# Performance work log

Hardware: AMD Instinct MI355X
Metric: run time of the kernel (lower is better)

The kernel has to match this reference:

```python
import jax, jax.numpy as jnp
import numpy as np

T, B, V, L = 512, 32, 512, 128
NEG = -1e9  # safe -inf surrogate (keeps logaddexp gradients finite)


def setup_inputs() -> dict:
    key = jax.random.key(0)
    k1, k2, k3 = jax.random.split(key, 3)
    log_probs = jax.nn.log_softmax(
        jax.random.normal(k1, (T, B, V), dtype=jnp.float32), axis=-1)
    # ASG transition parameter (init ones in the module; use small noise for a
    # non-degenerate reference). transition[i, j] = score of j -> i.
    transition = 0.1 * jax.random.normal(k2, (V, V), dtype=jnp.float32)
    targets = jax.random.randint(k3, (B, L), 0, V)
    input_lengths = jnp.full((B,), T, dtype=jnp.int32)
    target_lengths = jnp.full((B,), L, dtype=jnp.int32)
    return {"log_probs": log_probs, "transition": transition,
            "targets": targets, "input_lengths": input_lengths,
            "target_lengths": target_lengths}


def _fcc(log_probs, transition, input_lengths):
    """Fully-connected criterion: log-partition over all label paths. [B]"""
    def step(alpha, lp_t):  # alpha, lp_t: [B, V]
        # alpha'[b, i] = lp_t[b, i] + logsumexp_j(alpha[b, j] + trans[i, j])
        alpha = lp_t + jax.nn.logsumexp(
            alpha[:, None, :] + transition[None, :, :], axis=2)
        return alpha, jax.nn.logsumexp(alpha, axis=1)

    a0 = log_probs[0]
    _, tail = jax.lax.scan(step, a0, log_probs[1:])
    scores = jnp.concatenate(
        [jax.nn.logsumexp(a0, axis=1)[None], tail], axis=0)  # [T, B]
    return scores[input_lengths - 1, jnp.arange(scores.shape[1])]


def _fac(log_probs, transition, targets, input_lengths, target_lengths):
    """Forced-alignment criterion: DP constrained to the target label seq. [B]"""
    Tt, Bb, _ = log_probs.shape
    Ll = targets.shape[1]
    trans_self = transition[targets, targets]                    # [B, L] stay
    trans_prev = transition[targets[:, 1:], targets[:, :-1]]     # [B, L-1] advance
    # emit[t, b, s] = log_probs[t, b, targets[b, s]]
    emit = jnp.take_along_axis(
        log_probs, jnp.broadcast_to(targets[None], (Tt, Bb, Ll)), axis=2)

    sel = (target_lengths - 1)[:, None]  # [B, 1]

    def final_of(beta):
        return jnp.take_along_axis(beta, sel, axis=1)[:, 0]

    beta0 = jnp.where(jnp.arange(Ll)[None, :] == 0, emit[0], NEG)  # [B, L]

    def step(beta, em_t):
        stay = beta + trans_self
        move = jnp.concatenate(
            [jnp.full((Bb, 1), NEG, beta.dtype),
             beta[:, :-1] + trans_prev], axis=1)
        beta = em_t + jnp.logaddexp(stay, move)
        return beta, final_of(beta)

    _, tail = jax.lax.scan(step, beta0, emit[1:])
    fins = jnp.concatenate([final_of(beta0)[None], tail], axis=0)  # [T, B]
    return fins[input_lengths - 1, jnp.arange(Bb)]


def reference(log_probs, transition, targets, input_lengths, target_lengths):
    # ASG loss (reduction='none'): FCC - FAC, shape [B]
    fcc = _fcc(log_probs, transition, input_lengths)
    fac = _fac(log_probs, transition, targets, input_lengths, target_lengths)
    return fcc - fac
```

## Files before the change

kernel.cpp:

```cpp
#include <hip/hip_runtime.h>
#include <stdint.h>

#define T_ 512
#define B_ 32
#define V_ 512
#define L_ 128
#define NEGF (-1000000000.0f)

#define SE_Q 69.0f
#define SU_Q 127.0f
#define LOGC 9.078313f

template <int CTRL>
__device__ __forceinline__ int dppmov(int old_, int src) {
    return __builtin_amdgcn_update_dpp(old_, src, CTRL, 0xF, 0xF, false);
}
__device__ __forceinline__ float wave_max64(float x) {
    int xi = __float_as_int(x);
    x = fmaxf(x, __int_as_float(dppmov<0x111>(xi, xi))); xi = __float_as_int(x);
    x = fmaxf(x, __int_as_float(dppmov<0x112>(xi, xi))); xi = __float_as_int(x);
    x = fmaxf(x, __int_as_float(dppmov<0x114>(xi, xi))); xi = __float_as_int(x);
    x = fmaxf(x, __int_as_float(dppmov<0x118>(xi, xi))); xi = __float_as_int(x);
    x = fmaxf(x, __int_as_float(dppmov<0x142>(xi, xi))); xi = __float_as_int(x);
    x = fmaxf(x, __int_as_float(dppmov<0x143>(xi, xi)));
    return x;
}
__device__ __forceinline__ float wave_sum64(float x) {
    int xi = __float_as_int(x);
    x = x + __int_as_float(dppmov<0x111>(xi, xi)); xi = __float_as_int(x);
    x = x + __int_as_float(dppmov<0x112>(xi, xi)); xi = __float_as_int(x);
    x = x + __int_as_float(dppmov<0x114>(xi, xi)); xi = __float_as_int(x);
    x = x + __int_as_float(dppmov<0x118>(xi, xi)); xi = __float_as_int(x);
    x = x + __int_as_float(dppmov<0x142>(xi, xi)); xi = __float_as_int(x);
    x = x + __int_as_float(dppmov<0x143>(xi, xi));
    return x;
}
__device__ __forceinline__ unsigned fkey(float f) {
    unsigned u = __float_as_uint(f);
    return (u & 0x80000000u) ? ~u : (u | 0x80000000u);
}
__device__ __forceinline__ float funkey(unsigned k) {
    unsigned u = (k & 0x80000000u) ? (k ^ 0x80000000u) : ~k;
    return __uint_as_float(u);
}

__device__ __forceinline__ int gl_of(int lane) { return (lane & 3) | ((lane >> 1) & 4); }
__device__ __forceinline__ int g_of(int lane)  { return ((lane >> 2) & 1) | ((lane >> 3) & 6); }

__global__ void asg_prep(const float* __restrict__ trans, uint32_t* __restrict__ Et) {
    int o = blockIdx.x * blockDim.x + threadIdx.x;
    int d   = o & 3;
    int tid = (o >> 2) & 511;
    int q   = o >> 11;
    int w = tid >> 6, lane = tid & 63;
    int g = g_of(lane), gl = gl_of(lane);
    int c = q >> 2, kk = q & 3;
    int kp = (kk + (gl >> 1)) & 3;
    int m  = 4 * kp + d;
    int row = 64 * w + 8 * g + c;
    int j0  = 4 * (16 * gl + m);
    const float* tp = trans + (size_t)row * V_ + j0;
    uint32_t q0 = (uint32_t)fminf(127.0f, __expf(tp[0]) * SE_Q + 0.5f);
    uint32_t q1 = (uint32_t)fminf(127.0f, __expf(tp[1]) * SE_Q + 0.5f);
    uint32_t q2 = (uint32_t)fminf(127.0f, __expf(tp[2]) * SE_Q + 0.5f);
    uint32_t q3 = (uint32_t)fminf(127.0f, __expf(tp[3]) * SE_Q + 0.5f);
    Et[(size_t)o] = q0 | (q1 << 8) | (q2 << 16) | (q3 << 24);
}

__global__ __attribute__((amdgpu_flat_work_group_size(512, 512),
                          amdgpu_waves_per_eu(2, 2)))
void asg_main(
    const float* __restrict__ lp, const uint32_t* __restrict__ Et,
    const float* __restrict__ trans, const int* __restrict__ targets,
    const int* __restrict__ ilen, const int* __restrict__ tlen,
    float* __restrict__ fcc_ws, float* __restrict__ fac_ws)
{
    __shared__ float    facb[256];
    __shared__ __align__(16) uint32_t u_lds[128];
    __shared__ unsigned mslot[2];
    __shared__ float    sumf;

    const int bb  = blockIdx.x;
    const int tid = threadIdx.x;

    if (bb < B_) {
        const int b    = bb;
        const int lane = tid & 63;
        const int w    = tid >> 6;
        const int g    = g_of(lane);
        const int gl   = gl_of(lane);
        const int i    = 64 * w + 8 * g + gl;
        const int Tlen = ilen[b];
        const bool p0 = (lane & 1) != 0;
        const bool p1 = (lane & 2) != 0;
        const bool p3 = (lane & 8) != 0;

        int uaddr[4];
        #pragma unroll
        for (int kk = 0; kk < 4; ++kk)
            uaddr[kk] = 64 * gl + 16 * ((kk + (gl >> 1)) & 3);

        uint4 er4[32];
        {
            const uint4* Eq = (const uint4*)Et;
            #pragma unroll
            for (int q = 0; q < 32; ++q) er4[q] = Eq[q * 512 + tid];
        }

        float alpha = lp[(size_t)b * V_ + i];
        float lpv   = lp[(size_t)1 * (B_ * V_) + (size_t)b * V_ + i];
        if (tid == 511) { mslot[0] = 0u; mslot[1] = 0u; }
        __syncthreads();
        {
            float mx = wave_max64(alpha);
            if (lane == 63) atomicMax(&mslot[0], fkey(mx));
        }
        __syncthreads();
        float m = funkey(mslot[0]);

        for (int t = 1; t < Tlen; ++t) {
            {
                float u = __expf(alpha - m);
                uint32_t qu = (uint32_t)(u * SU_Q + 0.5f);
                int pv = (int)(qu << (8 * (i & 3)));
                pv |= dppmov<0xB1>(pv, pv);
                pv |= dppmov<0x4E>(pv, pv);
                if ((i & 3) == 0) u_lds[i >> 2] = (uint32_t)pv;
            }
            if (tid == 511) mslot[t & 1] = 0u;
            __syncthreads();

            int tn = (t + 1 < Tlen) ? (t + 1) : t;
            float lpv_n = lp[(size_t)tn * (B_ * V_) + (size_t)b * V_ + i];

            int acc0 = 0, acc1 = 0, acc2 = 0, acc3 = 0;
            int acc4 = 0, acc5 = 0, acc6 = 0, acc7 = 0;
            #pragma unroll
            for (int kk = 0; kk < 4; ++kk) {
                uint4 ub = *(const uint4*)((const char*)u_lds + uaddr[kk]);
                uint4 e;
                e = er4[0 * 4 + kk];
                acc0 = __builtin_amdgcn_sdot4((int)e.x, (int)ub.x, acc0, false);
                acc0 = __builtin_amdgcn_sdot4((int)e.y, (int)ub.y, acc0, false);
                acc0 = __builtin_amdgcn_sdot4((int)e.z, (int)ub.z, acc0, false);
                acc0 = __builtin_amdgcn_sdot4((int)e.w, (int)ub.w, acc0, false);
                e = er4[1 * 4 + kk];
                acc1 = __builtin_amdgcn_sdot4((int)e.x, (int)ub.x, acc1, false);
                acc1 = __builtin_amdgcn_sdot4((int)e.y, (int)ub.y, acc1, false);
                acc1 = __builtin_amdgcn_sdot4((int)e.z, (int)ub.z, acc1, false);
                acc1 = __builtin_amdgcn_sdot4((int)e.w, (int)ub.w, acc1, false);
                e = er4[2 * 4 + kk];
                acc2 = __builtin_amdgcn_sdot4((int)e.x, (int)ub.x, acc2, false);
                acc2 = __builtin_amdgcn_sdot4((int)e.y, (int)ub.y, acc2, false);
                acc2 = __builtin_amdgcn_sdot4((int)e.z, (int)ub.z, acc2, false);
                acc2 = __builtin_amdgcn_sdot4((int)e.w, (int)ub.w, acc2, false);
                e = er4[3 * 4 + kk];
                acc3 = __builtin_amdgcn_sdot4((int)e.x, (int)ub.x, acc3, false);
                acc3 = __builtin_amdgcn_sdot4((int)e.y, (int)ub.y, acc3, false);
                acc3 = __builtin_amdgcn_sdot4((int)e.z, (int)ub.z, acc3, false);
                acc3 = __builtin_amdgcn_sdot4((int)e.w, (int)ub.w, acc3, false);
                e = er4[4 * 4 + kk];
                acc4 = __builtin_amdgcn_sdot4((int)e.x, (int)ub.x, acc4, false);
                acc4 = __builtin_amdgcn_sdot4((int)e.y, (int)ub.y, acc4, false);
                acc4 = __builtin_amdgcn_sdot4((int)e.z, (int)ub.z, acc4, false);
                acc4 = __builtin_amdgcn_sdot4((int)e.w, (int)ub.w, acc4, false);
                e = er4[5 * 4 + kk];
                acc5 = __builtin_amdgcn_sdot4((int)e.x, (int)ub.x, acc5, false);
                acc5 = __builtin_amdgcn_sdot4((int)e.y, (int)ub.y, acc5, false);
                acc5 = __builtin_amdgcn_sdot4((int)e.z, (int)ub.z, acc5, false);
                acc5 = __builtin_amdgcn_sdot4((int)e.w, (int)ub.w, acc5, false);
                e = er4[6 * 4 + kk];
                acc6 = __builtin_amdgcn_sdot4((int)e.x, (int)ub.x, acc6, false);
                acc6 = __builtin_amdgcn_sdot4((int)e.y, (int)ub.y, acc6, false);
                acc6 = __builtin_amdgcn_sdot4((int)e.z, (int)ub.z, acc6, false);
                acc6 = __builtin_amdgcn_sdot4((int)e.w, (int)ub.w, acc6, false);
                e = er4[7 * 4 + kk];
                acc7 = __builtin_amdgcn_sdot4((int)e.x, (int)ub.x, acc7, false);
                acc7 = __builtin_amdgcn_sdot4((int)e.y, (int)ub.y, acc7, false);
                acc7 = __builtin_amdgcn_sdot4((int)e.z, (int)ub.z, acc7, false);
                acc7 = __builtin_amdgcn_sdot4((int)e.w, (int)ub.w, acc7, false);
            }

            int m0 = p0 ? acc1 : acc0;  int t0 = p0 ? acc0 : acc1;
            int m1 = p0 ? acc3 : acc2;  int t1 = p0 ? acc2 : acc3;
            int m2 = p0 ? acc5 : acc4;  int t2 = p0 ? acc4 : acc5;
            int m3 = p0 ? acc7 : acc6;  int t3 = p0 ? acc6 : acc7;
            m0 += dppmov<0xB1>(t0, t0);
            m1 += dppmov<0xB1>(t1, t1);
            m2 += dppmov<0xB1>(t2, t2);
            m3 += dppmov<0xB1>(t3, t3);
            int n0 = p1 ? m1 : m0;      int s0 = p1 ? m0 : m1;
            int n1 = p1 ? m3 : m2;      int s1 = p1 ? m2 : m3;
            n0 += dppmov<0x4E>(s0, s0);
            n1 += dppmov<0x4E>(s1, s1);
            int f0 = p3 ? n1 : n0;      int s2 = p3 ? n0 : n1;
            f0 += dppmov<0x128>(s2, s2);

            alpha = lpv + (m - LOGC) + __logf((float)f0);
            lpv = lpv_n;
            {
                float mx = wave_max64(alpha);
                if (lane == 63) atomicMax(&mslot[t & 1], fkey(mx));
            }
            __syncthreads();
            m = funkey(mslot[t & 1]);
        }

        if (tid == 511) sumf = 0.0f;
        __syncthreads();
        {
            float s = wave_sum64(__expf(alpha - m));
            if (lane == 63) atomicAdd(&sumf, s);
        }
        __syncthreads();
        if (tid == 0) fcc_ws[b] = m + __logf(sumf);
    } else {
        const int b = bb - B_;
        const int l = tid;
        const bool active = (l < L_);
        const int Tlen = ilen[b];
        const int Llen = tlen[b];

        const int tl  = active ? targets[b * L_ + l] : 0;
        const int tlm = (active && l > 0) ? targets[b * L_ + l - 1] : 0;
        const float ts = active ? trans[(size_t)tl * V_ + tl] : 0.0f;
        const float tp = (active && l > 0) ? trans[(size_t)tl * V_ + tlm] : 0.0f;

        float beta = (l == 0) ? lp[(size_t)b * V_ + tl] : NEGF;
        float em_next = active ? lp[(size_t)1 * (B_ * V_) + (size_t)b * V_ + tl] : 0.0f;

        for (int t = 1; t < Tlen; ++t) {
            float* buf = facb + (t & 1) * L_;
            if (active) buf[l] = beta;
            __syncthreads();
            float prev = (active && l > 0) ? buf[l - 1] : NEGF;
            float em = em_next;
            if (active && t + 1 < Tlen)
                em_next = lp[(size_t)(t + 1) * (B_ * V_) + (size_t)b * V_ + tl];
            if (active) {
                float st = beta + ts;
                float mv = prev + tp;
                float mx = fmaxf(st, mv);
                float mn = fminf(st, mv);
                beta = em + mx + log1pf(__expf(mn - mx));
            }
        }
        if (active && l == Llen - 1) fac_ws[b] = beta;
    }
}

__global__ void asg_combine(const float* __restrict__ fcc_ws,
                            const float* __restrict__ fac_ws,
                            float* __restrict__ out) {
    int i = threadIdx.x;
    if (i < B_) out[i] = fcc_ws[i] - fac_ws[i];
}

extern "C" void kernel_launch(void* const* d_in, const int* in_sizes, int n_in,
                              void* d_out, int out_size, void* d_ws, size_t ws_size,
                              hipStream_t stream) {
    const float* lp      = (const float*)d_in[0];
    const float* trans   = (const float*)d_in[1];
    const int*   targets = (const int*)d_in[2];
    const int*   ilen    = (const int*)d_in[3];
    const int*   tlen    = (const int*)d_in[4];
    float* out = (float*)d_out;

    uint32_t* Et     = (uint32_t*)d_ws;
    float*    fcc_ws = (float*)((char*)d_ws + 65536 * 4);
    float*    fac_ws = fcc_ws + B_;

    hipLaunchKernelGGL(asg_prep, dim3(256), dim3(256), 0, stream, trans, Et);
    hipLaunchKernelGGL(asg_main, dim3(2 * B_), dim3(512), 0, stream,
                       lp, Et, trans, targets, ilen, tlen, fcc_ws, fac_ws);
    hipLaunchKernelGGL(asg_combine, dim3(1), dim3(64), 0, stream, fcc_ws, fac_ws, out);
}
```

Before: 641.5 us.

## Use per-wave max with double-buffered LDS to halve barriers per FCC step

Each wave now normalizes its alpha slice by its own wave-local max instead of a block-wide max, and publishes that max to LDS alongside the quantized exponentials. Combined with double-buffered u_lds and max slots, this drops the second __syncthreads and the atomicMax per timestep, leaving one barrier per step. The consumer rescales each partial dot-product by exp(m_wave - m_block) in float before the reduction, so the DPP reduction moves from int to float adds. Per-wave quantization may change numerical error relative to a global max.

```diff
diff --git a/kernel.cpp b/kernel.cpp
--- a/kernel.cpp
+++ b/kernel.cpp
@@ -14,6 +14,11 @@
 template <int CTRL>
 __device__ __forceinline__ int dppmov(int old_, int src) {
     return __builtin_amdgcn_update_dpp(old_, src, CTRL, 0xF, 0xF, false);
+}
+template <int CTRL>
+__device__ __forceinline__ float dppfadd(float kept, float moved) {
+    int mi = __float_as_int(moved);
+    return kept + __int_as_float(dppmov<CTRL>(mi, mi));
 }
 __device__ __forceinline__ float wave_max64(float x) {
     int xi = __float_as_int(x);
@@ -76,8 +81,9 @@
     float* __restrict__ fcc_ws, float* __restrict__ fac_ws)
 {
     __shared__ float    facb[256];
-    __shared__ __align__(16) uint32_t u_lds[128];
-    __shared__ unsigned mslot[2];
+    __shared__ __align__(16) uint32_t u_lds[2][128];
+    __shared__ __align__(16) float    mwv[2][8];
+    __shared__ unsigned mslotE;
     __shared__ float    sumf;
 
     const int bb  = blockIdx.x;
@@ -109,35 +115,43 @@
 
         float alpha = lp[(size_t)b * V_ + i];
         float lpv   = lp[(size_t)1 * (B_ * V_) + (size_t)b * V_ + i];
-        if (tid == 511) { mslot[0] = 0u; mslot[1] = 0u; }
-        __syncthreads();
-        {
-            float mx = wave_max64(alpha);
-            if (lane == 63) atomicMax(&mslot[0], fkey(mx));
-        }
-        __syncthreads();
-        float m = funkey(mslot[0]);
+        if (tid == 511) { mslotE = 0u; sumf = 0.0f; }
 
         for (int t = 1; t < Tlen; ++t) {
+            const int buf = t & 1;
+
+            float mwx = wave_max64(alpha);
+            float mw  = __builtin_amdgcn_readlane(__float_as_int(mwx), 63) == 0
+                        ? 0.0f : 0.0f;
+            mw = __int_as_float(__builtin_amdgcn_readlane(__float_as_int(mwx), 63));
+
             {
-                float u = __expf(alpha - m);
+                float u = __expf(alpha - mw);
                 uint32_t qu = (uint32_t)(u * SU_Q + 0.5f);
                 int pv = (int)(qu << (8 * (i & 3)));
                 pv |= dppmov<0xB1>(pv, pv);
                 pv |= dppmov<0x4E>(pv, pv);
-                if ((i & 3) == 0) u_lds[i >> 2] = (uint32_t)pv;
+                if ((i & 3) == 0) u_lds[buf][i >> 2] = (uint32_t)pv;
             }
-            if (tid == 511) mslot[t & 1] = 0u;
-            __syncthreads();
+            if (lane == 63) mwv[buf][w] = mw;
 
             int tn = (t + 1 < Tlen) ? (t + 1) : t;
             float lpv_n = lp[(size_t)tn * (B_ * V_) + (size_t)b * V_ + i];
 
+            __syncthreads();
+
+            const float4* M4 = (const float4*)&mwv[buf][0];
+            float4 ma = M4[0], mc = M4[1];
+            float mglv = mwv[buf][gl];
+            float mb = fmaxf(fmaxf(fmaxf(ma.x, ma.y), fmaxf(ma.z, ma.w)),
+                             fmaxf(fmaxf(mc.x, mc.y), fmaxf(mc.z, mc.w)));
+
+            const char* ub_base = (const char*)&u_lds[buf][0];
             int acc0 = 0, acc1 = 0, acc2 = 0, acc3 = 0;
             int acc4 = 0, acc5 = 0, acc6 = 0, acc7 = 0;
             #pragma unroll
             for (int kk = 0; kk < 4; ++kk) {
-                uint4 ub = *(const uint4*)((const char*)u_lds + uaddr[kk]);
+                uint4 ub = *(const uint4*)(ub_base + uaddr[kk]);
                 uint4 e;
                 e = er4[0 * 4 + kk];
                 acc0 = __builtin_amdgcn_sdot4((int)e.x, (int)ub.x, acc0, false);
@@ -181,39 +195,43 @@
                 acc7 = __builtin_amdgcn_sdot4((int)e.w, (int)ub.w, acc7, false);
             }
 
-            int m0 = p0 ? acc1 : acc0;  int t0 = p0 ? acc0 : acc1;
-            int m1 = p0 ? acc3 : acc2;  int t1 = p0 ? acc2 : acc3;
-            int m2 = p0 ? acc5 : acc4;  int t2 = p0 ? acc4 : acc5;
-            int m3 = p0 ? acc7 : acc6;  int t3 = p0 ? acc6 : acc7;
-            m0 += dppmov<0xB1>(t0, t0);
-            m1 += dppmov<0xB1>(t1, t1);
-            m2 += dppmov<0xB1>(t2, t2);
-            m3 += dppmov<0xB1>(t3, t3);
-            int n0 = p1 ? m1 : m0;      int s0 = p1 ? m0 : m1;
-            int n1 = p1 ? m3 : m2;      int s1 = p1 ? m2 : m3;
-            n0 += dppmov<0x4E>(s0, s0);
-            n1 += dppmov<0x4E>(s1, s1);
-            int f0 = p3 ? n1 : n0;      int s2 = p3 ? n0 : n1;
-            f0 += dppmov<0x128>(s2, s2);
-
-            alpha = lpv + (m - LOGC) + __logf((float)f0);
+            float s = __expf(mglv - mb);
+            float fa0 = (float)acc0 * s, fa1 = (float)acc1 * s;
+            float fa2 = (float)acc2 * s, fa3 = (float)acc3 * s;
+            float fa4 = (float)acc4 * s, fa5 = (float)acc5 * s;
+            float fa6 = (float)acc6 * s, fa7 = (float)acc7 * s;
+
+            float A0 = p0 ? fa1 : fa0, B0 = p0 ? fa0 : fa1;
+            float A1 = p0 ? fa3 : fa2, B1 = p0 ? fa2 : fa3;
+            float A2 = p0 ? fa5 : fa4, B2 = p0 ? fa4 : fa5;
+            float A3 = p0 ? fa7 : fa6, B3 = p0 ? fa6 : fa7;
+            A0 = dppfadd<0xB1>(A0, B0);
+            A1 = dppfadd<0xB1>(A1, B1);
+            A2 = dppfadd<0xB1>(A2, B2);
+            A3 = dppfadd<0xB1>(A3, B3);
+            float C0 = p1 ? A1 : A0, D0 = p1 ? A0 : A1;
+            float C1 = p1 ? A3 : A2, D1 = p1 ? A2 : A3;
+            C0 = dppfadd<0x4E>(C0, D0);
+            C1 = dppfadd<0x4E>(C1, D1);
+            float F = p3 ? C1 : C0, G = p3 ? C0 : C1;
+            F = dppfadd<0x128>(F, G);
+
+            alpha = lpv + (mb - LOGC) + __logf(F);
             lpv = lpv_n;
-            {
-                float mx = wave_max64(alpha);
-                if (lane == 63) atomicMax(&mslot[t & 1], fkey(mx));
-            }
-            __syncthreads();
-            m = funkey(mslot[t & 1]);
-        }
-
-        if (tid == 511) sumf = 0.0f;
+        }
+
+        {
+            float mx = wave_max64(alpha);
+            if (lane == 63) atomicMax(&mslotE, fkey(mx));
+        }
         __syncthreads();
+        float m2 = funkey(mslotE);
         {
-            float s = wave_sum64(__expf(alpha - m));
-            if (lane == 63) atomicAdd(&sumf, s);
+            float sv = wave_sum64(__expf(alpha - m2));
+            if (lane == 63) atomicAdd(&sumf, sv);
         }
         __syncthreads();
-        if (tid == 0) fcc_ws[b] = m + __logf(sumf);
+        if (tid == 0) fcc_ws[b] = m2 + __logf(sumf);
     } else {
         const int b = bb - B_;
         const int l = tid;
```

New measurement: 621.5 us. -3.1%, faster.
